# Optimization experiments

Measured on AMD Instinct MI355X. Metric: run time of the kernel, lower is better.

## Reference

```python
import jax, jax.numpy as jnp
import numpy as np

N_HEADS = 16

def setup_inputs() -> dict:
    key = jax.random.key(0)
    k1, k2, k3, k4, k5 = jax.random.split(key, 5)
    B, S, D = 2, 2048, 1024
    x = jax.random.normal(k1, (B, S, D), dtype=jnp.float32)
    # parameters scaled ~ fan-in to keep softmax logits sane
    w_in = jax.random.normal(k2, (D, 3 * D), dtype=jnp.float32) * (1.0 / np.sqrt(D))
    b_in = jax.random.normal(k3, (3 * D,), dtype=jnp.float32) * 0.02
    w_out = jax.random.normal(k4, (D, D), dtype=jnp.float32) * (1.0 / np.sqrt(D))
    b_out = jax.random.normal(k5, (D,), dtype=jnp.float32) * 0.02
    return {"x": x, "w_in": w_in, "b_in": b_in, "w_out": w_out, "b_out": b_out,
            "causal_mask": 1}


def reference(x, w_in, b_in, w_out, b_out, causal_mask):
    B, S, D = x.shape
    H = N_HEADS
    dh = D // H
    qkv = x @ w_in + b_in                        # [B, S, 3D]
    q, k, v = jnp.split(qkv, 3, axis=-1)          # each [B, S, D]
    q = q.reshape(B, S, H, dh)
    k = k.reshape(B, S, H, dh)
    v = v.reshape(B, S, H, dh)
    # scores: [B, H, Sq, Sk]
    scores = jnp.einsum("bqhd,bkhd->bhqk", q, k)
    if causal_mask:
        mask = jnp.triu(jnp.ones((S, S), dtype=bool), k=1)
        scores = jnp.where(mask, -jnp.inf, scores)
    scores = scores / jnp.sqrt(jnp.asarray(dh, dtype=scores.dtype))
    weight = jax.nn.softmax(scores, axis=-1)
    out = jnp.einsum("bhqk,bkhd->bqhd", weight, v).reshape(B, S, D)
    return out @ w_out + b_out
```

## Files before the change

### kernel.cpp

```cpp
#include <hip/hip_runtime.h>
#include <hip/hip_bf16.h>

typedef __attribute__((ext_vector_type(8))) short short8;
typedef __attribute__((ext_vector_type(4))) short s16x4;
typedef __attribute__((ext_vector_type(4))) float f32x4;
typedef unsigned short u16;

__device__ inline u16 f2bf(float f) {
    union { float f; unsigned u; } x{f};
    unsigned r = (x.u + 0x7fff + ((x.u >> 16) & 1)) >> 16;
    return (u16)r;
}

__device__ inline unsigned pkbf(float hi, float lo) {
    unsigned a = __builtin_bit_cast(unsigned, hi) + 0x8000u;
    unsigned b = __builtin_bit_cast(unsigned, lo) + 0x8000u;
    return __builtin_amdgcn_perm(a, b, 0x07060302u);
}

__device__ inline void glds16(const u16* g, u16* l) {
    __builtin_amdgcn_global_load_lds(
        (const __attribute__((address_space(1))) void*)g,
        (__attribute__((address_space(3))) void*)l, 16, 0, 0);
}

__global__ __launch_bounds__(256) void prep(const float* __restrict__ x,
                                            const float* __restrict__ w_in,
                                            const float* __restrict__ w_out,
                                            u16* __restrict__ Xb,
                                            u16* __restrict__ WtIn,
                                            u16* __restrict__ WtOut) {
    __shared__ float tile[32][33];
    int bx = blockIdx.x, tid = threadIdx.x;
    if (bx < 4096) {
        int i = (bx * 256 + tid) * 4;
        float4 v = *(const float4*)&x[i];
        uint2 o;
        o.x = (unsigned)f2bf(v.x) | ((unsigned)f2bf(v.y) << 16);
        o.y = (unsigned)f2bf(v.z) | ((unsigned)f2bf(v.w) << 16);
        *(uint2*)&Xb[i] = o;
        return;
    }
    const float* W; u16* Wt; int K, N, n0, k0;
    if (bx < 7168) {
        int b2 = bx - 4096;
        W = w_in; Wt = WtIn; K = 1024; N = 3072;
        n0 = (b2 % 96) * 32; k0 = (b2 / 96) * 32;
    } else {
        int b3 = bx - 7168;
        W = w_out; Wt = WtOut; K = 1024; N = 1024;
        n0 = (b3 & 31) * 32; k0 = (b3 >> 5) * 32;
    }
    int tx = tid & 31, ty = tid >> 5;
    for (int i = 0; i < 32; i += 8)
        tile[ty + i][tx] = W[(size_t)(k0 + ty + i) * N + n0 + tx];
    __syncthreads();
    for (int i = 0; i < 32; i += 8)
        Wt[(size_t)(n0 + ty + i) * K + k0 + tx] = f2bf(tile[tx][ty + i]);
}

__global__ __launch_bounds__(256) void transpose_v(const u16* __restrict__ qkv,
                                                   u16* __restrict__ VT) {
    __shared__ u16 t[32][33];
    int s0 = blockIdx.x * 32, d0 = blockIdx.y * 32, bh = blockIdx.z;
    int b = bh >> 4, h = bh & 15;
    int tx = threadIdx.x, ty = threadIdx.y;
    const u16* Vp = qkv + (size_t)(b * 2048) * 3072 + 2048 + h * 64;
    for (int i = 0; i < 32; i += 8)
        t[ty + i][tx] = Vp[(size_t)(s0 + ty + i) * 3072 + d0 + tx];
    __syncthreads();
    u16* Vr = VT + (size_t)bh * 64 * 2048;
    for (int i = 0; i < 32; i += 8)
        Vr[(size_t)(d0 + ty + i) * 2048 + s0 + tx] = t[tx][ty + i];
}

#define BM 128
#define BN 128
#define BK 64
__global__ __launch_bounds__(256) void gemm_bt(const u16* __restrict__ A,
                                               const u16* __restrict__ Bt,
                                               const float* __restrict__ bias,
                                               void* __restrict__ C,
                                               int M, int N, int K, int c_is_f32,
                                               int qcols, float qscale) {
    __shared__ u16 smem[2 * BM * BK + 2048];
    u16* As = smem;
    u16* Bs = smem + BM * BK;

    int tid = threadIdx.x;
    int wave = tid >> 6, lane = tid & 63;
    int quad = lane >> 4, l16 = lane & 15;
    int wm = (wave >> 1) * 64, wn = (wave & 1) * 64;

    int nm = M / BM, nn = N / BN;
    const int GM = 8;
    int per_group = GM * nn;
    int group = blockIdx.x / per_group;
    int rem = blockIdx.x % per_group;
    int first_m = group * GM;
    int gsz = (nm - first_m < GM) ? (nm - first_m) : GM;
    int m0 = (first_m + rem % gsz) * BM;
    int n0 = (rem / gsz) * BN;

    f32x4 acc[4][4] = {};

    for (int k0 = 0; k0 < K; k0 += BK) {
        __syncthreads();
        for (int i = 0; i < 4; i++) {
            int c = tid + i * 256;
            int r = c >> 3, cc = c & 7;
            int gsrc = (cc ^ (r & 7)) * 8;
            glds16(&A[(size_t)(m0 + r) * K + k0 + gsrc], As + c * 8);
            glds16(&Bt[(size_t)(n0 + r) * K + k0 + gsrc], Bs + c * 8);
        }
        __syncthreads();
        for (int ks = 0; ks < 2; ks++) {
            short8 af[4], bf[4];
            for (int i = 0; i < 4; i++) {
                int row = wm + i * 16 + l16;
                int slot = (ks * 4 + quad) ^ (row & 7);
                af[i] = *(short8*)&As[row * BK + slot * 8];
            }
            for (int j = 0; j < 4; j++) {
                int row = wn + j * 16 + l16;
                int slot = (ks * 4 + quad) ^ (row & 7);
                bf[j] = *(short8*)&Bs[row * BK + slot * 8];
            }
            for (int i = 0; i < 4; i++)
                for (int j = 0; j < 4; j++)
                    acc[i][j] = __builtin_amdgcn_mfma_f32_16x16x32_bf16(
                        af[i], bf[j], acc[i][j], 0, 0, 0);
        }
    }

    if (c_is_f32) {
        for (int i = 0; i < 4; i++)
            for (int j = 0; j < 4; j++) {
                int col = n0 + wn + j * 16 + l16;
                float bv = bias ? bias[col] : 0.f;
                for (int r = 0; r < 4; r++) {
                    int row = m0 + wm + i * 16 + quad * 4 + r;
                    ((float*)C)[(size_t)row * N + col] = acc[i][j][r] + bv;
                }
            }
    } else {
        __syncthreads();
        u16 (*buf)[136] = (u16(*)[136])smem;
        for (int i = 0; i < 4; i++)
            for (int j = 0; j < 4; j++) {
                int col = wn + j * 16 + l16;
                float bv = bias ? bias[n0 + col] : 0.f;
                float scl = (n0 + col < qcols) ? qscale : 1.f;
                for (int r = 0; r < 4; r++)
                    buf[wm + i * 16 + quad * 4 + r][col] =
                        f2bf((acc[i][j][r] + bv) * scl);
            }
        __syncthreads();
        u16* Cb = (u16*)C;
        for (int it = 0; it < 8; it++) {
            int c = tid + it * 256;
            int row = c >> 4, k8 = c & 15;
            uint4 v = *(uint4*)&buf[row][k8 * 8];
            *(uint4*)&Cb[(size_t)(m0 + row) * N + n0 + k8 * 8] = v;
        }
    }
}

__global__ __launch_bounds__(256, 2) void attn_kernel(const u16* __restrict__ qkv,
                                                      const u16* __restrict__ VT,
                                                      u16* __restrict__ out) {
    const int S = 2048, D = 1024, stride = 3072;
    int idx = blockIdx.x;
    int slot = idx >> 8;
    int r5 = idx & 255;
    int p = r5 >> 5, bh = r5 & 31;
    int qt = slot ? p : 15 - p;
    int b = bh >> 4, h = bh & 15;
    int tid = threadIdx.x;
    int wave = tid >> 6, lane = tid & 63;
    int quad = lane >> 4, l16 = lane & 15;

    __shared__ u16 Klds[2][2][64 * 64];
    __shared__ u16 Vlds[2][2][64 * 64];

    const u16* Qp = qkv + (size_t)(b * S) * stride + h * 64;
    const u16* Kp = Qp + D;
    const u16* Vtp = VT + (size_t)bh * 64 * S;

    short8 qf[2][2];
    for (int qh = 0; qh < 2; qh++) {
        int qrow = qt * 128 + wave * 32 + qh * 16 + l16;
        qf[qh][0] = *(const short8*)&Qp[(size_t)qrow * stride + quad * 8];
        qf[qh][1] = *(const short8*)&Qp[(size_t)qrow * stride + 32 + quad * 8];
    }

    auto stage = [&](int kt, int bsel, int ch) {
        for (int i = 0; i < 2; i++) {
            int c = tid + i * 256;
            int rr = c >> 3, cc = c & 7;
            int gsrc = (cc ^ (rr & 7)) * 8;
            glds16(&Kp[(size_t)(kt * 64 + rr) * stride + gsrc],
                   &Klds[bsel][ch][c * 8]);
            glds16(&Vtp[(size_t)rr * S + kt * 64 + gsrc],
                   &Vlds[bsel][ch][c * 8]);
        }
    };

    stage(0, 0, 0);
    stage(1, 0, 1);

    f32x4 O[4][2] = {};
    float ls[2] = {0.f, 0.f};

    int np = qt + 1;
    for (int j = 0; j < np; j++) {
        int cur = j & 1;
        __syncthreads();
        if (j + 1 < np) {
            stage(2 * (j + 1), cur ^ 1, 0);
            stage(2 * (j + 1) + 1, cur ^ 1, 1);
        }
        bool last = (j == qt);

        s16x4 pf[2][2][4];
        for (int ch = 0; ch < 2; ch++) {
            short8 kf[4][2];
            for (int nb = 0; nb < 4; nb++) {
                int rr = nb * 16 + l16;
                int s0 = ((0 + quad) ^ (rr & 7)) * 8;
                int s1 = ((4 + quad) ^ (rr & 7)) * 8;
                kf[nb][0] = *(short8*)&Klds[cur][ch][rr * 64 + s0];
                kf[nb][1] = *(short8*)&Klds[cur][ch][rr * 64 + s1];
            }
            for (int qh = 0; qh < 2; qh++) {
                f32x4 st[4];
                for (int nb = 0; nb < 4; nb++) {
                    f32x4 t = {};
                    t = __builtin_amdgcn_mfma_f32_16x16x32_bf16(
                        kf[nb][0], qf[qh][0], t, 0, 0, 0);
                    t = __builtin_amdgcn_mfma_f32_16x16x32_bf16(
                        kf[nb][1], qf[qh][1], t, 0, 0, 0);
                    st[nb] = t;
                }
                if (last) {
                    int qabs = qt * 128 + wave * 32 + qh * 16 + l16;
                    for (int nb = 0; nb < 4; nb++) {
                        int kb0 = (2 * j + ch) * 64 + nb * 16 + quad * 4;
                        for (int r = 0; r < 4; r++) {
                            float e = __builtin_amdgcn_exp2f(st[nb][r]);
                            st[nb][r] = (kb0 + r <= qabs) ? e : 0.f;
                        }
                    }
                } else {
                    for (int nb = 0; nb < 4; nb++)
                        for (int r = 0; r < 4; r++)
                            st[nb][r] = __builtin_amdgcn_exp2f(st[nb][r]);
                }
                for (int nb = 0; nb < 4; nb++) {
                    ls[qh] += (st[nb][0] + st[nb][1]) + (st[nb][2] + st[nb][3]);
                    uint2 pk;
                    pk.x = pkbf(st[nb][1], st[nb][0]);
                    pk.y = pkbf(st[nb][3], st[nb][2]);
                    pf[ch][qh][nb] = __builtin_bit_cast(s16x4, pk);
                }
            }
        }

        for (int db = 0; db < 4; db++) {
            int rr = db * 16 + l16;
            for (int kc = 0; kc < 4; kc++) {
                int g = kc * 2 + (quad >> 1);
                int sl = g ^ (rr & 7);
                int off = rr * 64 + sl * 8 + (quad & 1) * 4;
                s16x4 vfa = *(s16x4*)&Vlds[cur][0][off];
                s16x4 vfb = *(s16x4*)&Vlds[cur][1][off];
                for (int qh = 0; qh < 2; qh++) {
                    O[db][qh] = __builtin_amdgcn_mfma_f32_16x16x16bf16_1k(
                        vfa, pf[0][qh][kc], O[db][qh], 0, 0, 0);
                    O[db][qh] = __builtin_amdgcn_mfma_f32_16x16x16bf16_1k(
                        vfb, pf[1][qh][kc], O[db][qh], 0, 0, 0);
                }
            }
        }
    }

    for (int qh = 0; qh < 2; qh++) {
        float v = ls[qh];
        v += __shfl_xor(v, 16);
        v += __shfl_xor(v, 32);
        float rinv = 1.f / v;
        int qrow = qt * 128 + wave * 32 + qh * 16 + l16;
        for (int db = 0; db < 4; db++) {
            uint2 o;
            o.x = pkbf(O[db][qh][1] * rinv, O[db][qh][0] * rinv);
            o.y = pkbf(O[db][qh][3] * rinv, O[db][qh][2] * rinv);
            *(uint2*)&out[(size_t)(b * S + qrow) * D + h * 64 + db * 16 +
                          quad * 4] = o;
        }
    }
}

extern "C" void kernel_launch(void* const* d_in, const int* in_sizes, int n_in,
                              void* d_out, int out_size, void* d_ws, size_t ws_size,
                              hipStream_t stream) {
    const float* x     = (const float*)d_in[0];
    const float* w_in  = (const float*)d_in[1];
    const float* b_in  = (const float*)d_in[2];
    const float* w_out = (const float*)d_in[3];
    const float* b_out = (const float*)d_in[4];

    const int Bsz = 2, S = 2048, D = 1024, H = 16;
    const int M = Bsz * S;
    const int N1 = 3 * D;
    const float sc = 0.125f * 1.44269504f;

    u16* ws    = (u16*)d_ws;
    u16* Xb    = ws;
    u16* WtIn  = Xb + (size_t)M * D;
    u16* WtOut = WtIn + (size_t)N1 * D;
    u16* qkvb  = WtOut + (size_t)D * D;
    u16* attnb = qkvb + (size_t)M * N1;
    u16* Vt    = Xb;

    prep<<<8192, 256, 0, stream>>>(x, w_in, w_out, Xb, WtIn, WtOut);
    gemm_bt<<<(M / BM) * (N1 / BN), 256, 0, stream>>>(Xb, WtIn, b_in, qkvb,
                                                      M, N1, D, 0, D, sc);
    transpose_v<<<dim3(S / 32, 2, Bsz * H), dim3(32, 8), 0, stream>>>(qkvb, Vt);
    attn_kernel<<<512, 256, 0, stream>>>(qkvb, Vt, attnb);
    gemm_bt<<<(M / BM) * (D / BN), 256, 0, stream>>>(attnb, WtOut, b_out, d_out,
                                                     M, D, D, 1, 0, 1.f);
}
```

Before: 184.3 us.

## Software-pipeline attention QK/softmax/PV across chunks and shrink output GEMM tile

The attention inner loop is split into qk, softmax and pv stages for the two 64-key chunks and reordered so that chunk 1's QK MFMAs and chunk 0's PV MFMAs are issued around the softmax work. s_setprio raises wave priority around the matrix phases so other waves' exp work can interleave with them. Separately, gemm_bt is templated on tile size and the output projection uses 64x128 tiles, giving 512 blocks instead of 256 for better occupancy of the CUs. The risks are higher register pressure from keeping both score buffers live, and lower data reuse per block in the smaller GEMM tile.

```diff
diff --git a/kernel.cpp b/kernel.cpp
--- a/kernel.cpp
+++ b/kernel.cpp
@@ -74,68 +74,73 @@
         Vr[(size_t)(d0 + ty + i) * 2048 + s0 + tx] = t[tx][ty + i];
 }
 
-#define BM 128
-#define BN 128
 #define BK 64
+template<int TBM, int TBN>
 __global__ __launch_bounds__(256) void gemm_bt(const u16* __restrict__ A,
                                                const u16* __restrict__ Bt,
                                                const float* __restrict__ bias,
                                                void* __restrict__ C,
                                                int M, int N, int K, int c_is_f32,
                                                int qcols, float qscale) {
-    __shared__ u16 smem[2 * BM * BK + 2048];
+    __shared__ u16 smem[TBM * BK + TBN * BK + 2048];
     u16* As = smem;
-    u16* Bs = smem + BM * BK;
+    u16* Bs = smem + TBM * BK;
 
     int tid = threadIdx.x;
     int wave = tid >> 6, lane = tid & 63;
     int quad = lane >> 4, l16 = lane & 15;
-    int wm = (wave >> 1) * 64, wn = (wave & 1) * 64;
-
-    int nm = M / BM, nn = N / BN;
+    int wm = (wave >> 1) * (TBM / 2), wn = (wave & 1) * (TBN / 2);
+    constexpr int MI = TBM / 32, NJ = TBN / 32;
+
+    int nm = M / TBM, nn = N / TBN;
     const int GM = 8;
     int per_group = GM * nn;
     int group = blockIdx.x / per_group;
     int rem = blockIdx.x % per_group;
     int first_m = group * GM;
     int gsz = (nm - first_m < GM) ? (nm - first_m) : GM;
-    int m0 = (first_m + rem % gsz) * BM;
-    int n0 = (rem / gsz) * BN;
-
-    f32x4 acc[4][4] = {};
+    int m0 = (first_m + rem % gsz) * TBM;
+    int n0 = (rem / gsz) * TBN;
+
+    f32x4 acc[MI][NJ] = {};
 
     for (int k0 = 0; k0 < K; k0 += BK) {
         __syncthreads();
-        for (int i = 0; i < 4; i++) {
+        for (int i = 0; i < TBM * 8 / 256; i++) {
             int c = tid + i * 256;
             int r = c >> 3, cc = c & 7;
             int gsrc = (cc ^ (r & 7)) * 8;
             glds16(&A[(size_t)(m0 + r) * K + k0 + gsrc], As + c * 8);
+        }
+        for (int i = 0; i < TBN * 8 / 256; i++) {
+            int c = tid + i * 256;
+            int r = c >> 3, cc = c & 7;
+            int gsrc = (cc ^ (r & 7)) * 8;
             glds16(&Bt[(size_t)(n0 + r) * K + k0 + gsrc], Bs + c * 8);
         }
         __syncthreads();
         for (int ks = 0; ks < 2; ks++) {
-            short8 af[4], bf[4];
-            for (int i = 0; i < 4; i++) {
+            short8 af[MI], bf[NJ];
+            for (int i = 0; i < MI; i++) {
                 int row = wm + i * 16 + l16;
                 int slot = (ks * 4 + quad) ^ (row & 7);
                 af[i] = *(short8*)&As[row * BK + slot * 8];
             }
-            for (int j = 0; j < 4; j++) {
+            for (int j = 0; j < NJ; j++) {
                 int row = wn + j * 16 + l16;
                 int slot = (ks * 4 + quad) ^ (row & 7);
                 bf[j] = *(short8*)&Bs[row * BK + slot * 8];
             }
-            for (int i = 0; i < 4; i++)
-                for (int j = 0; j < 4; j++)
+            for (int i = 0; i < MI; i++)
+                for (int j = 0; j < NJ; j++)
                     acc[i][j] = __builtin_amdgcn_mfma_f32_16x16x32_bf16(
                         af[i], bf[j], acc[i][j], 0, 0, 0);
         }
     }
 
     if (c_is_f32) {
-        for (int i = 0; i < 4; i++)
-            for (int j = 0; j < 4; j++) {
+        for (int i = 0; i < MI; i++)
+            for (int j = 0; j < NJ; j++) {
                 int col = n0 + wn + j * 16 + l16;
                 float bv = bias ? bias[col] : 0.f;
                 for (int r = 0; r < 4; r++) {
@@ -146,8 +151,8 @@
     } else {
         __syncthreads();
         u16 (*buf)[136] = (u16(*)[136])smem;
-        for (int i = 0; i < 4; i++)
-            for (int j = 0; j < 4; j++) {
+        for (int i = 0; i < MI; i++)
+            for (int j = 0; j < NJ; j++) {
                 int col = wn + j * 16 + l16;
                 float bv = bias ? bias[n0 + col] : 0.f;
                 float scl = (n0 + col < qcols) ? qscale : 1.f;
@@ -157,9 +162,9 @@
             }
         __syncthreads();
         u16* Cb = (u16*)C;
-        for (int it = 0; it < 8; it++) {
+        for (int it = 0; it < TBM * 16 / 256; it++) {
             int c = tid + it * 256;
-            int row = c >> 4, k8 = c & 15;
+            int row = c / (TBN / 8), k8 = c % (TBN / 8);
             uint4 v = *(uint4*)&buf[row][k8 * 8];
             *(uint4*)&Cb[(size_t)(m0 + row) * N + n0 + k8 * 8] = v;
         }
@@ -222,8 +227,7 @@
         }
         bool last = (j == qt);
 
-        s16x4 pf[2][2][4];
-        for (int ch = 0; ch < 2; ch++) {
+        auto qk = [&](int ch, f32x4 st[2][4]) {
             short8 kf[4][2];
             for (int nb = 0; nb < 4; nb++) {
                 int rr = nb * 16 + l16;
@@ -232,56 +236,72 @@
                 kf[nb][0] = *(short8*)&Klds[cur][ch][rr * 64 + s0];
                 kf[nb][1] = *(short8*)&Klds[cur][ch][rr * 64 + s1];
             }
-            for (int qh = 0; qh < 2; qh++) {
-                f32x4 st[4];
+            for (int qh = 0; qh < 2; qh++)
                 for (int nb = 0; nb < 4; nb++) {
                     f32x4 t = {};
                     t = __builtin_amdgcn_mfma_f32_16x16x32_bf16(
                         kf[nb][0], qf[qh][0], t, 0, 0, 0);
                     t = __builtin_amdgcn_mfma_f32_16x16x32_bf16(
                         kf[nb][1], qf[qh][1], t, 0, 0, 0);
-                    st[nb] = t;
-                }
+                    st[qh][nb] = t;
+                }
+        };
+        auto sm = [&](int ch, f32x4 st[2][4], s16x4 pfc[2][4]) {
+            for (int qh = 0; qh < 2; qh++) {
                 if (last) {
                     int qabs = qt * 128 + wave * 32 + qh * 16 + l16;
                     for (int nb = 0; nb < 4; nb++) {
                         int kb0 = (2 * j + ch) * 64 + nb * 16 + quad * 4;
                         for (int r = 0; r < 4; r++) {
-                            float e = __builtin_amdgcn_exp2f(st[nb][r]);
-                            st[nb][r] = (kb0 + r <= qabs) ? e : 0.f;
+                            float e = __builtin_amdgcn_exp2f(st[qh][nb][r]);
+                            st[qh][nb][r] = (kb0 + r <= qabs) ? e : 0.f;
                         }
                     }
                 } else {
                     for (int nb = 0; nb < 4; nb++)
                         for (int r = 0; r < 4; r++)
-                            st[nb][r] = __builtin_amdgcn_exp2f(st[nb][r]);
+                            st[qh][nb][r] = __builtin_amdgcn_exp2f(st[qh][nb][r]);
                 }
                 for (int nb = 0; nb < 4; nb++) {
-                    ls[qh] += (st[nb][0] + st[nb][1]) + (st[nb][2] + st[nb][3]);
+                    ls[qh] += (st[qh][nb][0] + st[qh][nb][1]) +
+                              (st[qh][nb][2] + st[qh][nb][3]);
                     uint2 pk;
-                    pk.x = pkbf(st[nb][1], st[nb][0]);
-                    pk.y = pkbf(st[nb][3], st[nb][2]);
-                    pf[ch][qh][nb] = __builtin_bit_cast(s16x4, pk);
-                }
-            }
-        }
-
-        for (int db = 0; db < 4; db++) {
-            int rr = db * 16 + l16;
-            for (int kc = 0; kc < 4; kc++) {
-                int g = kc * 2 + (quad >> 1);
-                int sl = g ^ (rr & 7);
-                int off = rr * 64 + sl * 8 + (quad & 1) * 4;
-                s16x4 vfa = *(s16x4*)&Vlds[cur][0][off];
-                s16x4 vfb = *(s16x4*)&Vlds[cur][1][off];
-                for (int qh = 0; qh < 2; qh++) {
-                    O[db][qh] = __builtin_amdgcn_mfma_f32_16x16x16bf16_1k(
-                        vfa, pf[0][qh][kc], O[db][qh], 0, 0, 0);
-                    O[db][qh] = __builtin_amdgcn_mfma_f32_16x16x16bf16_1k(
-                        vfb, pf[1][qh][kc], O[db][qh], 0, 0, 0);
-                }
-            }
-        }
+                    pk.x = pkbf(st[qh][nb][1], st[qh][nb][0]);
+                    pk.y = pkbf(st[qh][nb][3], st[qh][nb][2]);
+                    pfc[qh][nb] = __builtin_bit_cast(s16x4, pk);
+                }
+            }
+        };
+        auto pv = [&](int ch, s16x4 pfc[2][4]) {
+            for (int db = 0; db < 4; db++) {
+                int rr = db * 16 + l16;
+                for (int kc = 0; kc < 4; kc++) {
+                    int g = kc * 2 + (quad >> 1);
+                    int sl = g ^ (rr & 7);
+                    int off = rr * 64 + sl * 8 + (quad & 1) * 4;
+                    s16x4 vf = *(s16x4*)&Vlds[cur][ch][off];
+                    for (int qh = 0; qh < 2; qh++)
+                        O[db][qh] = __builtin_amdgcn_mfma_f32_16x16x16bf16_1k(
+                            vf, pfc[qh][kc], O[db][qh], 0, 0, 0);
+                }
+            }
+        };
+
+        f32x4 stA[2][4], stB[2][4];
+        s16x4 pfA[2][4], pfB[2][4];
+
+        __builtin_amdgcn_s_setprio(1);
+        qk(0, stA);
+        __builtin_amdgcn_s_setprio(0);
+        sm(0, stA, pfA);
+        __builtin_amdgcn_s_setprio(1);
+        qk(1, stB);
+        pv(0, pfA);
+        __builtin_amdgcn_s_setprio(0);
+        sm(1, stB, pfB);
+        __builtin_amdgcn_s_setprio(1);
+        pv(1, pfB);
+        __builtin_amdgcn_s_setprio(0);
     }
 
     for (int qh = 0; qh < 2; qh++) {
@@ -323,10 +343,10 @@
     u16* Vt    = Xb;
 
     prep<<<8192, 256, 0, stream>>>(x, w_in, w_out, Xb, WtIn, WtOut);
-    gemm_bt<<<(M / BM) * (N1 / BN), 256, 0, stream>>>(Xb, WtIn, b_in, qkvb,
-                                                      M, N1, D, 0, D, sc);
+    gemm_bt<128, 128><<<(M / 128) * (N1 / 128), 256, 0, stream>>>(
+        Xb, WtIn, b_in, qkvb, M, N1, D, 0, D, sc);
     transpose_v<<<dim3(S / 32, 2, Bsz * H), dim3(32, 8), 0, stream>>>(qkvb, Vt);
     attn_kernel<<<512, 256, 0, stream>>>(qkvb, Vt, attnb);
-    gemm_bt<<<(M / BM) * (D / BN), 256, 0, stream>>>(attnb, WtOut, b_out, d_out,
-                                                     M, D, D, 1, 0, 1.f);
-}
+    gemm_bt<64, 128><<<(M / 64) * (D / 128), 256, 0, stream>>>(
+        attnb, WtOut, b_out, d_out, M, D, D, 1, 0, 1.f);
+}
```

After: 179.1 us. -2.8%, faster.
